# Performance work log

Measured on AMD Instinct MI355X. Metric: run time of the kernel, lower is better.

The kernel has to match this reference:

```python
import jax, jax.numpy as jnp
import numpy as np


def setup_inputs() -> dict:
    key = jax.random.key(0)
    k1, k2 = jax.random.split(key)
    B, C, H, W, K = 8, 32, 224, 224, 5
    x = jax.random.normal(k1, (B, C, H, W), dtype=jnp.float32)
    kernel = jax.random.normal(k2, (C, 1, K, K), dtype=jnp.float32) * 0.1
    return {"x": x, "kernel": kernel, "stride": 1, "padding": 2, "dilation": 1}


def reference(x, kernel, stride, padding, dilation):
    # Tropical-max (morphological dilation) conv: out[p] = max_k (x[p+k] + w_flipped[k]).
    # is_max=True, softmax_temp=None -> hard max; kernel is flipped (true convolution).
    B, C, H, W = x.shape
    OC, _, K, _ = kernel.shape
    neutral = -jnp.inf
    x_pad = jnp.pad(x, ((0, 0), (0, 0), (padding, padding), (padding, padding)),
                    constant_values=neutral)
    Hp, Wp = H + 2 * padding, W + 2 * padding
    H_out = (Hp - dilation * (K - 1) - 1) // stride + 1
    W_out = (Wp - dilation * (K - 1) - 1) // stride + 1
    wflip = kernel[:, 0, ::-1, ::-1]  # (C, K, K) flipped, as in torch kernel.flip((2,3))
    # Start from neutral: matches the extra neutral row padded onto the unfold tensor.
    out = jnp.full((B, C, H_out, W_out), neutral, dtype=x.dtype)
    for i in range(K):  # small fixed K*K loop; avoids materializing the (B,C,K^2,HW) unfold
        for j in range(K):
            patch = x_pad[:, :,
                          i * dilation: i * dilation + (H_out - 1) * stride + 1: stride,
                          j * dilation: j * dilation + (W_out - 1) * stride + 1: stride]
            out = jnp.maximum(out, patch + wflip[:, i, j][None, :, None, None])
    return out
```

## Files before the change

### kernel.cpp

```cpp
#include <hip/hip_runtime.h>
#include <math.h>


#define TC_B 8
#define TC_C 32
#define TC_H 224
#define TC_W 224
#define TC_WQ 56
#define TC_HG 14

__device__ __forceinline__ float4 sel4(bool ok, float4 v, float n) {
  return make_float4(ok ? v.x : n, ok ? v.y : n, ok ? v.z : n, ok ? v.w : n);
}

__global__ __launch_bounds__(256) void tropical_conv2d_kernel(
    const float* __restrict__ x, const float* __restrict__ kern,
    float* __restrict__ out) {
  const int tid = threadIdx.x;
  const int wq = tid & 63;
  const int yl = tid >> 6;
  const int blk = blockIdx.x;
  const int hg = blk % TC_HG;
  const int bc = blk / TC_HG;
  const int c = bc & (TC_C - 1);

  if (wq >= TC_WQ) return;

  const int hbase = hg * 16 + yl * 4;
  const float* xp = x + (size_t)bc * (TC_H * TC_W);
  const float NEG = -INFINITY;

  const int wqm1 = (wq > 0) ? wq - 1 : 0;
  const int wqp1 = (wq < TC_WQ - 1) ? wq + 1 : TC_WQ - 1;
  const bool lok = (wq > 0);
  const bool rok = (wq < TC_WQ - 1);

  float4 rA[8], rB[8], rC[8];
  #pragma unroll
  for (int i = 0; i < 8; ++i) {
    const int rr = hbase - 2 + i;
    const int rc = rr < 0 ? 0 : (rr > TC_H - 1 ? TC_H - 1 : rr);
    const float4* row = (const float4*)(xp + (size_t)rc * TC_W);
    rA[i] = row[wqm1];
    rB[i] = row[wq];
    rC[i] = row[wqp1];
  }

  float w[25];
  #pragma unroll
  for (int q = 0; q < 25; ++q) w[q] = kern[c * 25 + 24 - q];

  #pragma unroll
  for (int i = 0; i < 8; ++i) {
    const int rr = hbase - 2 + i;
    const bool rowok = (rr >= 0) && (rr < TC_H);
    rA[i] = sel4(rowok && lok, rA[i], NEG);
    rB[i] = sel4(rowok, rB[i], NEG);
    rC[i] = sel4(rowok && rok, rC[i], NEG);
  }

  float acc[4][4];
  #pragma unroll
  for (int o = 0; o < 4; ++o)
    #pragma unroll
    for (int k = 0; k < 4; ++k) acc[o][k] = NEG;

  #pragma unroll
  for (int ri = 0; ri < 8; ++ri) {
    const float v[12] = {rA[ri].x, rA[ri].y, rA[ri].z, rA[ri].w,
                         rB[ri].x, rB[ri].y, rB[ri].z, rB[ri].w,
                         rC[ri].x, rC[ri].y, rC[ri].z, rC[ri].w};
    #pragma unroll
    for (int o = 0; o < 4; ++o) {
      const int i = ri - o;
      if (i < 0 || i > 4) continue;
      #pragma unroll
      for (int k = 0; k < 4; ++k) {
        const float t0 = v[2 + k] + w[i * 5 + 0];
        const float t1 = v[3 + k] + w[i * 5 + 1];
        const float t2 = v[4 + k] + w[i * 5 + 2];
        const float t3 = v[5 + k] + w[i * 5 + 3];
        const float t4 = v[6 + k] + w[i * 5 + 4];
        acc[o][k] = fmaxf(fmaxf(fmaxf(acc[o][k], t0), t1),
                          fmaxf(fmaxf(t2, t3), t4));
      }
    }
  }

  float* op = out + (size_t)bc * (TC_H * TC_W) + (size_t)hbase * TC_W;
  #pragma unroll
  for (int o = 0; o < 4; ++o) {
    ((float4*)(op + (size_t)o * TC_W))[wq] =
        make_float4(acc[o][0], acc[o][1], acc[o][2], acc[o][3]);
  }
}

extern "C" void kernel_launch(void* const* d_in, const int* in_sizes, int n_in,
                              void* d_out, int out_size, void* d_ws, size_t ws_size,
                              hipStream_t stream) {
  const float* x = (const float*)d_in[0];
  const float* k = (const float*)d_in[1];
  float* out = (float*)d_out;

  dim3 block(256, 1, 1);
  dim3 grid(TC_B * TC_C * TC_HG, 1, 1);
  tropical_conv2d_kernel<<<grid, block, 0, stream>>>(x, k, out);
}
```

Measured before the change: 118.8 us.

## Stage input rows in LDS via global_load_lds instead of redundant register loads

Replaces per-thread redundant global loads (each thread fetched 8 rows × 3 float4s, with halo overlap across threads and row groups) with a cooperative tile of 20 rows loaded once into shared memory using the direct global-to-LDS load builtin. Threads then read their 3 float4 neighbours per row from LDS, with -inf padding columns and a right-edge mask handling borders. This is meant to cut duplicate global and L2 traffic, at the cost of a block-wide barrier, LDS usage and extra LDS reads.

```diff
diff --git a/kernel.cpp b/kernel.cpp
--- a/kernel.cpp
+++ b/kernel.cpp
@@ -8,56 +8,54 @@
 #define TC_W 224
 #define TC_WQ 56
 #define TC_HG 14
-
-__device__ __forceinline__ float4 sel4(bool ok, float4 v, float n) {
-  return make_float4(ok ? v.x : n, ok ? v.y : n, ok ? v.z : n, ok ? v.w : n);
-}
+#define T_ROWS 20
+#define ROW_F4 65
+#define ROW_FL (ROW_F4 * 4)
 
 __global__ __launch_bounds__(256) void tropical_conv2d_kernel(
     const float* __restrict__ x, const float* __restrict__ kern,
     float* __restrict__ out) {
   const int tid = threadIdx.x;
-  const int wq = tid & 63;
+  const int lane = tid & 63;
   const int yl = tid >> 6;
   const int blk = blockIdx.x;
   const int hg = blk % TC_HG;
   const int bc = blk / TC_HG;
   const int c = bc & (TC_C - 1);
 
-  if (wq >= TC_WQ) return;
+  __shared__ float tile[T_ROWS * ROW_FL];
 
-  const int hbase = hg * 16 + yl * 4;
+  const float NEG = -INFINITY;
+  const float4 NINF4 = make_float4(NEG, NEG, NEG, NEG);
   const float* xp = x + (size_t)bc * (TC_H * TC_W);
-  const float NEG = -INFINITY;
 
-  const int wqm1 = (wq > 0) ? wq - 1 : 0;
-  const int wqp1 = (wq < TC_WQ - 1) ? wq + 1 : TC_WQ - 1;
-  const bool lok = (wq > 0);
-  const bool rok = (wq < TC_WQ - 1);
+  if (tid < T_ROWS) *(float4*)&tile[tid * ROW_FL] = NINF4;
 
-  float4 rA[8], rB[8], rC[8];
+  const int cl = lane < TC_WQ ? lane : TC_WQ - 1;
   #pragma unroll
-  for (int i = 0; i < 8; ++i) {
-    const int rr = hbase - 2 + i;
-    const int rc = rr < 0 ? 0 : (rr > TC_H - 1 ? TC_H - 1 : rr);
-    const float4* row = (const float4*)(xp + (size_t)rc * TC_W);
-    rA[i] = row[wqm1];
-    rB[i] = row[wq];
-    rC[i] = row[wqp1];
+  for (int rr = 0; rr < 5; ++rr) {
+    const int r = yl * 5 + rr;
+    const int g = hg * 16 - 2 + r;
+    float* ldsrow = &tile[r * ROW_FL + 4];
+    if (g >= 0 && g < TC_H) {
+      const float* gp = xp + (size_t)g * TC_W + cl * 4;
+      __builtin_amdgcn_global_load_lds(
+          (const __attribute__((address_space(1))) void*)gp,
+          (__attribute__((address_space(3))) void*)ldsrow, 16, 0, 0);
+    } else {
+      *(float4*)(ldsrow + (size_t)lane * 4) = NINF4;
+    }
   }
 
   float w[25];
   #pragma unroll
   for (int q = 0; q < 25; ++q) w[q] = kern[c * 25 + 24 - q];
 
-  #pragma unroll
-  for (int i = 0; i < 8; ++i) {
-    const int rr = hbase - 2 + i;
-    const bool rowok = (rr >= 0) && (rr < TC_H);
-    rA[i] = sel4(rowok && lok, rA[i], NEG);
-    rB[i] = sel4(rowok, rB[i], NEG);
-    rC[i] = sel4(rowok && rok, rC[i], NEG);
-  }
+  __syncthreads();
+
+  if (lane >= TC_WQ) return;
+
+  const int hbase = hg * 16 + yl * 4;
 
   float acc[4][4];
   #pragma unroll
@@ -65,11 +63,19 @@
     #pragma unroll
     for (int k = 0; k < 4; ++k) acc[o][k] = NEG;
 
+  const bool redge = (lane == TC_WQ - 1);
+
   #pragma unroll
   for (int ri = 0; ri < 8; ++ri) {
-    const float v[12] = {rA[ri].x, rA[ri].y, rA[ri].z, rA[ri].w,
-                         rB[ri].x, rB[ri].y, rB[ri].z, rB[ri].w,
-                         rC[ri].x, rC[ri].y, rC[ri].z, rC[ri].w};
+    const float* rp = &tile[(yl * 4 + ri) * ROW_FL + 4 * lane];
+    const float4 A = *(const float4*)(rp);
+    const float4 Bv = *(const float4*)(rp + 4);
+    const float4 Cv = *(const float4*)(rp + 8);
+    float v[12] = {A.x, A.y, A.z, A.w, Bv.x, Bv.y, Bv.z, Bv.w,
+                   Cv.x, Cv.y, Cv.z, Cv.w};
+    v[8] = redge ? NEG : v[8];
+    v[9] = redge ? NEG : v[9];
+
     #pragma unroll
     for (int o = 0; o < 4; ++o) {
       const int i = ri - o;
@@ -90,7 +96,7 @@
   float* op = out + (size_t)bc * (TC_H * TC_W) + (size_t)hbase * TC_W;
   #pragma unroll
   for (int o = 0; o < 4; ++o) {
-    ((float4*)(op + (size_t)o * TC_W))[wq] =
+    ((float4*)(op + (size_t)o * TC_W))[lane] =
         make_float4(acc[o][0], acc[o][1], acc[o][2], acc[o][3]);
   }
 }
```

Result: faster. 108.8 us (-8.4%).
